# Kernel tuning notes

Hardware: AMD Instinct MI355X
Metric: run time of the kernel (lower is better)

Reference implementation:

```python
import jax, jax.numpy as jnp
import numpy as np

DEPTH = 2
DIM = 1024     # shot-embedding width
SDIM = 256     # SSM state width
B = 256        # batch (episodes x classes)
S = 64         # shots per class (scan length)
EPS = 1e-5


def setup_inputs() -> dict:
    key = jax.random.key(0)
    ks = jax.random.split(key, 10)
    sc = 0.02
    return {
        "shot_embeddings": jax.random.normal(ks[0], (B, S, DIM), jnp.float32),
        # per-layer selective-scan cell params (stacked over depth)
        "Wd": jax.random.normal(ks[1], (DEPTH, DIM, SDIM), jnp.float32) * sc,   # delta proj
        "bd": jnp.zeros((DEPTH, SDIM), jnp.float32),
        "Wi": jax.random.normal(ks[2], (DEPTH, DIM, SDIM), jnp.float32) * sc,   # input (B) proj
        "bi": jnp.zeros((DEPTH, SDIM), jnp.float32),
        "A_log": jax.random.normal(ks[3], (DEPTH, SDIM), jnp.float32),          # state decay param
        "Wo": jax.random.normal(ks[4], (DEPTH, SDIM, DIM), jnp.float32) * sc,   # readout (C) proj
        "bo": jnp.zeros((DEPTH, DIM), jnp.float32),
        # state_to_class Linear(state_dim, dim) per layer
        "Ws": jax.random.normal(ks[5], (DEPTH, SDIM, DIM), jnp.float32) * sc,
        "bs": jnp.zeros((DEPTH, DIM), jnp.float32),
        # LayerNorm
        "gamma": jnp.ones((DIM,), jnp.float32),
        "beta": jnp.zeros((DIM,), jnp.float32),
    }


def _run_selective_scan(x, Wd, bd, Wi, bi, A_log, Wo, bo):
    """Mamba-style selective scan over the shot axis.
    x: [B,S,D] -> (y: [B,S,D], final_state: [B,N])"""
    delta = jax.nn.softplus(jnp.einsum('bsd,dn->bsn', x, Wd) + bd)   # [B,S,N]
    u = jnp.einsum('bsd,dn->bsn', x, Wi) + bi                        # [B,S,N]
    decay = jnp.exp(-delta * jax.nn.softplus(A_log))                 # [B,S,N]
    drive = delta * u                                                # [B,S,N]

    def step(h, t):
        d, g = t
        h = d * h + g
        return h, h

    h0 = jnp.zeros((x.shape[0], Wd.shape[1]), x.dtype)
    final, hs = jax.lax.scan(step, h0, (decay.swapaxes(0, 1), drive.swapaxes(0, 1)))
    hs = hs.swapaxes(0, 1)                                           # [B,S,N]
    y = jnp.einsum('bsn,nd->bsd', hs, Wo) + bo                       # [B,S,D]
    return y, final


def reference(shot_embeddings, Wd, bd, Wi, bi, A_log, Wo, bo, Ws, bs, gamma, beta):
    hidden = shot_embeddings
    class_state = None
    for l in range(Wd.shape[0]):  # fixed small depth
        hidden, state = _run_selective_scan(hidden, Wd[l], bd[l], Wi[l], bi[l],
                                            A_log[l], Wo[l], bo[l])
        class_state = jnp.einsum('bn,nd->bd', state, Ws[l]) + bs[l]   # [B,D]
        hidden = hidden + class_state[:, None, :]
    pooled = class_state + hidden.mean(axis=1)                        # [B,D]
    mu = pooled.mean(axis=-1, keepdims=True)
    var = pooled.var(axis=-1, keepdims=True)
    class_repr = (pooled - mu) / jnp.sqrt(var + EPS) * gamma + beta
    return class_repr, hidden
```

## Files before the change

### kernel.cpp

```cpp
#include <hip/hip_runtime.h>
#include <hip/hip_bf16.h>

#define DEPTH 2
#define DIM   1024
#define SDIM  256
#define BATCH 256
#define SHOTS 64
#define M_TOT (BATCH*SHOTS)
#define SGRP  4
#define GSTEP (SHOTS/SGRP)

typedef __attribute__((ext_vector_type(8))) short bf16x8;
typedef __attribute__((ext_vector_type(4))) float f32x4;
typedef unsigned short u16;

__device__ __forceinline__ u16 f2bf(float f) {
    union { float f; unsigned u; } v; v.f = f;
    unsigned r = v.u + 0x7fffu + ((v.u >> 16) & 1u);
    return (u16)(r >> 16);
}

__device__ __forceinline__ unsigned pk_bf2(float a, float b) {
    union { __hip_bfloat162 h2; unsigned u; } c;
    c.h2 = __float22bfloat162_rn(make_float2(a, b));
    return c.u;
}

__device__ __forceinline__ float softplus_f(float x) {
    if (x > 20.f) return x;
    return log1pf(__expf(x));
}

__device__ __forceinline__ void gld16(const u16* g, u16* l) {
    __builtin_amdgcn_global_load_lds(
        (const __attribute__((address_space(1))) unsigned int*)g,
        (__attribute__((address_space(3))) unsigned int*)l, 16, 0, 0);
}

__global__ __launch_bounds__(256)
void transpose_conv(const float* __restrict__ A1, const float* __restrict__ A2,
                    u16* __restrict__ out, int K, int N, int SPLIT)
{
    __shared__ float T[64][65];
    const int layer = blockIdx.z;
    const int k0 = blockIdx.x * 64, n0 = blockIdx.y * 64;
    const int tid = threadIdx.x;

    const bool first = (n0 < SPLIT);
    const int scols = first ? SPLIT : (N - SPLIT);
    const float* S = (first ? A1 : A2) + (size_t)layer * K * scols
                     + (first ? n0 : (n0 - SPLIT));
    out += (size_t)layer * K * N;

    #pragma unroll
    for (int i = 0; i < 4; ++i) {
        const int c = tid + i * 256;
        const int kr = c >> 4, cc = c & 15;
        const float4 v = *(const float4*)(S + (size_t)(k0 + kr) * scols + cc * 4);
        T[kr][cc * 4 + 0] = v.x; T[kr][cc * 4 + 1] = v.y;
        T[kr][cc * 4 + 2] = v.z; T[kr][cc * 4 + 3] = v.w;
    }
    __syncthreads();
    #pragma unroll
    for (int i = 0; i < 4; ++i) {
        const int c = tid + i * 256;
        const int nr = c >> 4, cc = c & 15;
        ushort4 h;
        h.x = f2bf(T[cc * 4 + 0][nr]); h.y = f2bf(T[cc * 4 + 1][nr]);
        h.z = f2bf(T[cc * 4 + 2][nr]); h.w = f2bf(T[cc * 4 + 3][nr]);
        *(ushort4*)&out[(size_t)(n0 + nr) * K + k0 + cc * 4] = h;
    }
}

__global__ __launch_bounds__(256)
void conv_bf16(const float* __restrict__ in, u16* __restrict__ out)
{
    const size_t total = (size_t)M_TOT * DIM;
    const size_t stride = (size_t)gridDim.x * 256 * 8;
    for (size_t i = ((size_t)blockIdx.x * 256 + threadIdx.x) * 8; i < total; i += stride) {
        const float4 a = *(const float4*)(in + i);
        const float4 b = *(const float4*)(in + i + 4);
        int4 o;
        o.x = (int)pk_bf2(a.x, a.y); o.y = (int)pk_bf2(a.z, a.w);
        o.z = (int)pk_bf2(b.x, b.y); o.w = (int)pk_bf2(b.z, b.w);
        *(int4*)(out + i) = o;
    }
}

#define BM 128
#define BN 128
#define BK 32

template<int EPI, bool SWIZ, bool BF16OUT, bool POOL>
__global__ __launch_bounds__(256)
void gemm_bf16(const u16* __restrict__ A, const u16* __restrict__ BT,
               void* __restrict__ Cv, const float* __restrict__ bo,
               const float* __restrict__ cs, float* __restrict__ pooled,
               int K, int ldc, int CB)
{
    __shared__ __align__(16) u16 As[BM * BK];
    __shared__ __align__(16) u16 Bs[BN * BK];

    const int tid = threadIdx.x;
    const int id  = blockIdx.x;
    int rb, cb;
    if (SWIZ) {
        const int xcd = id & 7, slot = id >> 3;
        rb = xcd + 8 * (slot / CB);
        cb = slot % CB;
    } else {
        rb = id / CB; cb = id % CB;
    }
    const int row0 = rb * BM, col0 = cb * BN;

    const int l  = tid & 63;
    const int w  = tid >> 6;
    const int wm = (w >> 1) * 64, wn = (w & 1) * 64;
    const int lr = l & 15, lq = l >> 4;

    const int sg   = w * 2;
    const int srow = l >> 2;
    const int scol = (l & 3) * 8;
    const u16* Ag = A  + (size_t)(row0 + sg * 16 + srow) * K + scol;
    const u16* Bg = BT + (size_t)(col0 + sg * 16 + srow) * K + scol;
    u16* Asd = &As[sg * 512 + l * 8];
    u16* Bsd = &Bs[sg * 512 + l * 8];

    f32x4 acc[4][4];
    #pragma unroll
    for (int i = 0; i < 4; ++i)
        #pragma unroll
        for (int j = 0; j < 4; ++j)
            acc[i][j] = (f32x4){0.f, 0.f, 0.f, 0.f};

    for (int k0 = 0; k0 < K; k0 += BK) {
        gld16(Ag + k0,                  Asd);
        gld16(Ag + (size_t)16 * K + k0, Asd + 512);
        gld16(Bg + k0,                  Bsd);
        gld16(Bg + (size_t)16 * K + k0, Bsd + 512);
        __syncthreads();

        bf16x8 af[4], bfr[4];
        #pragma unroll
        for (int i = 0; i < 4; ++i)
            af[i] = *(const bf16x8*)&As[(wm + i * 16 + lr) * BK + lq * 8];
        #pragma unroll
        for (int j = 0; j < 4; ++j)
            bfr[j] = *(const bf16x8*)&Bs[(wn + j * 16 + lr) * BK + lq * 8];

        #pragma unroll
        for (int i = 0; i < 4; ++i)
            #pragma unroll
            for (int j = 0; j < 4; ++j)
                acc[i][j] = __builtin_amdgcn_mfma_f32_16x16x32_bf16(
                    af[i], bfr[j], acc[i][j], 0, 0, 0);
        __syncthreads();
    }

    float psum[4] = {0.f, 0.f, 0.f, 0.f};
    #pragma unroll
    for (int i = 0; i < 4; ++i) {
        const int grow = row0 + wm + i * 16 + lq * 4;
        #pragma unroll
        for (int j = 0; j < 4; ++j) {
            const int gcol = col0 + wn + j * 16 + lr;
            float addv = 0.f;
            if (EPI >= 1) addv += bo[gcol];
            if (EPI == 2) addv += cs[(size_t)(grow >> 6) * DIM + gcol];
            #pragma unroll
            for (int r = 0; r < 4; ++r) {
                const float val = acc[i][j][r] + addv;
                if (BF16OUT) ((u16*)Cv)[(size_t)(grow + r) * ldc + gcol] = f2bf(val);
                else         ((float*)Cv)[(size_t)(grow + r) * ldc + gcol] = val;
                if (POOL) psum[j] += val;
            }
        }
    }
    if (POOL) {
        const int batch_w = (row0 + wm) >> 6;
        #pragma unroll
        for (int j = 0; j < 4; ++j) {
            float v = psum[j];
            v += __shfl_xor(v, 16, 64);
            v += __shfl_xor(v, 32, 64);
            if (lq == 0)
                pooled[(size_t)batch_w * DIM + col0 + wn + j * 16 + lr] = v;
        }
    }
}

__global__ __launch_bounds__(512, 8)
void scan_batch(const float* __restrict__ PQ,
                const float* __restrict__ bd, const float* __restrict__ bi,
                const float* __restrict__ A_log,
                u16* __restrict__ hsb, u16* __restrict__ stateb)
{
    const int b  = blockIdx.x;
    const int nc = threadIdx.x & 127;
    const int n  = nc + (blockIdx.y << 7);
    const int g  = threadIdx.x >> 7;
    const float bdv = bd[n], biv = bi[n];
    const float spA = softplus_f(A_log[n]);
    const size_t m0 = (size_t)b * SHOTS + g * GSTEP;
    const float* base = PQ + m0 * 512 + n;

    float dec[GSTEP], drv[GSTEP];
    #pragma unroll
    for (int s = 0; s < GSTEP; ++s) {
        dec[s] = base[s * 512];
        drv[s] = base[s * 512 + SDIM];
    }
    float a = 1.f, hl = 0.f;
    #pragma unroll
    for (int s = 0; s < GSTEP; ++s) {
        const float delta = softplus_f(dec[s] + bdv);
        const float d  = __expf(-delta * spA);
        const float gv = delta * (drv[s] + biv);
        dec[s] = d; drv[s] = gv;
        a *= d; hl = d * hl + gv;
    }

    __shared__ float2 grp[SGRP][128];
    grp[g][nc] = make_float2(a, hl);
    __syncthreads();

    float h = 0.f;
    for (int j = 0; j < g; ++j) {
        const float2 sv = grp[j][nc];
        h = sv.x * h + sv.y;
    }

    u16* hout = hsb + m0 * SDIM + n;
    #pragma unroll
    for (int s = 0; s < GSTEP; ++s) {
        h = dec[s] * h + drv[s];
        hout[s * SDIM] = f2bf(h);
    }
    if (g == SGRP - 1) stateb[(size_t)b * SDIM + n] = f2bf(h);
}

__global__ __launch_bounds__(1024)
void final_kernel(const float* __restrict__ pooled, const float* __restrict__ cs,
                  const float* __restrict__ gamma, const float* __restrict__ beta,
                  float* __restrict__ out)
{
    const int b = blockIdx.x;
    const int d = threadIdx.x;

    const float p = cs[(size_t)b * DIM + d]
                  + pooled[(size_t)b * DIM + d] * (1.f / SHOTS);

    __shared__ float rsum[1024], rsq[1024];
    rsum[d] = p; rsq[d] = p * p;
    __syncthreads();
    for (int off = 512; off > 0; off >>= 1) {
        if (d < off) { rsum[d] += rsum[d + off]; rsq[d] += rsq[d + off]; }
        __syncthreads();
    }
    const float mu  = rsum[0] * (1.f / DIM);
    const float var = rsq[0] * (1.f / DIM) - mu * mu;
    const float inv = rsqrtf(var + 1e-5f);

    out[(size_t)b * DIM + d] = (p - mu) * inv * gamma[d] + beta[d];
}


extern "C" void kernel_launch(void* const* d_in, const int* in_sizes, int n_in,
                              void* d_out, int out_size, void* d_ws, size_t ws_size,
                              hipStream_t stream)
{
    const float* X0    = (const float*)d_in[0];
    const float* Wd    = (const float*)d_in[1];
    const float* bd    = (const float*)d_in[2];
    const float* Wi    = (const float*)d_in[3];
    const float* bi    = (const float*)d_in[4];
    const float* A_log = (const float*)d_in[5];
    const float* Wo    = (const float*)d_in[6];
    const float* bo    = (const float*)d_in[7];
    const float* Ws    = (const float*)d_in[8];
    const float* bs    = (const float*)d_in[9];
    const float* gamma = (const float*)d_in[10];
    const float* beta  = (const float*)d_in[11];

    float* out_cr     = (float*)d_out;
    float* out_hidden = out_cr + (size_t)BATCH * DIM;

    u16* Xbf = (u16*)out_hidden;

    char* w = (char*)d_ws;
    float*  PQ     = (float*)w;  w += (size_t)M_TOT * 512 * 4;
    float*  csbuf  = (float*)w;  w += (size_t)BATCH * DIM * 4;
    float*  pooled = (float*)w;  w += (size_t)BATCH * DIM * 4;
    u16*    stateb = (u16*)w;    w += (size_t)BATCH * SDIM * 2;
    u16*    hsb    = (u16*)w;    w += (size_t)M_TOT * SDIM * 2;
    u16*    WcombT = (u16*)w;    w += (size_t)DEPTH * 512 * 1024 * 2;
    u16*    WoT    = (u16*)w;    w += (size_t)DEPTH * 1024 * 256 * 2;
    u16*    WsT    = (u16*)w;    w += (size_t)DEPTH * 1024 * 256 * 2;

    transpose_conv<<<dim3(1024 / 64, 512 / 64, DEPTH), 256, 0, stream>>>(
        Wd, Wi, WcombT, 1024, 512, 256);
    transpose_conv<<<dim3(256 / 64, 1024 / 64, DEPTH), 256, 0, stream>>>(
        Wo, Wo, WoT, 256, 1024, 1024);
    transpose_conv<<<dim3(256 / 64, 1024 / 64, DEPTH), 256, 0, stream>>>(
        Ws, Ws, WsT, 256, 1024, 1024);
    conv_bf16<<<2048, 256, 0, stream>>>(X0, Xbf);

    for (int l = 0; l < DEPTH; ++l) {
        gemm_bf16<0, true, false, false><<<512, 256, 0, stream>>>(
            Xbf, WcombT + (size_t)l * 512 * 1024, PQ, nullptr, nullptr, nullptr,
            1024, 512, 4);
        scan_batch<<<dim3(BATCH, 2), 512, 0, stream>>>(
            PQ, bd + l * SDIM, bi + l * SDIM, A_log + l * SDIM, hsb, stateb);
        gemm_bf16<1, false, false, false><<<16, 256, 0, stream>>>(
            stateb, WsT + (size_t)l * 1024 * 256, csbuf, bs + l * DIM, nullptr,
            nullptr, 256, 1024, 8);
        if (l < DEPTH - 1) {
            gemm_bf16<2, true, true, false><<<1024, 256, 0, stream>>>(
                hsb, WoT + (size_t)l * 1024 * 256, Xbf, bo + l * DIM, csbuf,
                nullptr, 256, 1024, 8);
        } else {
            gemm_bf16<2, true, false, true><<<1024, 256, 0, stream>>>(
                hsb, WoT + (size_t)l * 1024 * 256, out_hidden, bo + l * DIM, csbuf,
                pooled, 256, 1024, 8);
        }
    }
    final_kernel<<<BATCH, 1024, 0, stream>>>(pooled, csbuf, gamma, beta, out_cr);
}
```

Before: 299.7 us.

## Fuse state-to-class projection into scan kernel and merge prep kernels

Merges the three weight transpose kernels and the input bf16 conversion into a single prep launch. The scan kernel now runs one 1024-thread block per batch item covering all 256 state channels, keeps the final state in shared memory, and computes the state-to-class projection with a scalar dot product over a bf16 copy of Ws. This removes the small 16-block GEMM launch, the stateb round trip and several launches. The cost is that each scan block serially reads a 256x1024 bf16 weight slab, and the scan grid halves, so per-block scalar FMA work and lower parallelism may offset the saved launches.

```diff
diff --git a/kernel.cpp b/kernel.cpp
--- a/kernel.cpp
+++ b/kernel.cpp
@@ -26,6 +26,10 @@
     return c.u;
 }
 
+__device__ __forceinline__ float bf2f(u16 h) {
+    union { unsigned u; float f; } c; c.u = (unsigned)h << 16; return c.f;
+}
+
 __device__ __forceinline__ float softplus_f(float x) {
     if (x > 20.f) return x;
     return log1pf(__expf(x));
@@ -37,15 +41,11 @@
         (__attribute__((address_space(3))) unsigned int*)l, 16, 0, 0);
 }
 
-__global__ __launch_bounds__(256)
-void transpose_conv(const float* __restrict__ A1, const float* __restrict__ A2,
-                    u16* __restrict__ out, int K, int N, int SPLIT)
-{
-    __shared__ float T[64][65];
-    const int layer = blockIdx.z;
-    const int k0 = blockIdx.x * 64, n0 = blockIdx.y * 64;
-    const int tid = threadIdx.x;
-
+__device__ __forceinline__ void transpose_body(
+    float T[64][65], const float* __restrict__ A1, const float* __restrict__ A2,
+    u16* __restrict__ out, int K, int N, int SPLIT, int k0, int n0, int layer,
+    int tid)
+{
     const bool first = (n0 < SPLIT);
     const int scols = first ? SPLIT : (N - SPLIT);
     const float* S = (first ? A1 : A2) + (size_t)layer * K * scols
@@ -73,17 +73,42 @@
 }
 
 __global__ __launch_bounds__(256)
-void conv_bf16(const float* __restrict__ in, u16* __restrict__ out)
-{
-    const size_t total = (size_t)M_TOT * DIM;
-    const size_t stride = (size_t)gridDim.x * 256 * 8;
-    for (size_t i = ((size_t)blockIdx.x * 256 + threadIdx.x) * 8; i < total; i += stride) {
-        const float4 a = *(const float4*)(in + i);
-        const float4 b = *(const float4*)(in + i + 4);
+void prep(const float* __restrict__ Wd, const float* __restrict__ Wi,
+          const float* __restrict__ Wo, const float* __restrict__ Ws,
+          const float* __restrict__ X0,
+          u16* __restrict__ WcombT, u16* __restrict__ WoT,
+          u16* __restrict__ Wsb, u16* __restrict__ Xbf)
+{
+    __shared__ float T[64][65];
+    const int bid = blockIdx.x;
+    const int tid = threadIdx.x;
+
+    if (bid < 256) {
+        const int kx = bid & 15, ny = (bid >> 4) & 7, lz = bid >> 7;
+        transpose_body(T, Wd, Wi, WcombT, 1024, 512, 256, kx * 64, ny * 64, lz, tid);
+    } else if (bid < 384) {
+        const int sub = bid - 256;
+        const int kx = sub & 3, ny = (sub >> 2) & 15, lz = sub >> 6;
+        transpose_body(T, Wo, Wo, WoT, 256, 1024, 1024, kx * 64, ny * 64, lz, tid);
+    } else if (bid < 640) {
+        const size_t i = ((size_t)(bid - 384) * 256 + tid) * 8;
+        const float4 a = *(const float4*)(Ws + i);
+        const float4 b = *(const float4*)(Ws + i + 4);
         int4 o;
         o.x = (int)pk_bf2(a.x, a.y); o.y = (int)pk_bf2(a.z, a.w);
         o.z = (int)pk_bf2(b.x, b.y); o.w = (int)pk_bf2(b.z, b.w);
-        *(int4*)(out + i) = o;
+        *(int4*)(Wsb + i) = o;
+    } else {
+        const size_t total = (size_t)M_TOT * DIM;
+        const size_t stride = (size_t)2048 * 256 * 8;
+        for (size_t i = ((size_t)(bid - 640) * 256 + tid) * 8; i < total; i += stride) {
+            const float4 a = *(const float4*)(X0 + i);
+            const float4 b = *(const float4*)(X0 + i + 4);
+            int4 o;
+            o.x = (int)pk_bf2(a.x, a.y); o.y = (int)pk_bf2(a.z, a.w);
+            o.z = (int)pk_bf2(b.x, b.y); o.w = (int)pk_bf2(b.z, b.w);
+            *(int4*)(Xbf + i) = o;
+        }
     }
 }
 
@@ -189,16 +214,16 @@
     }
 }
 
-__global__ __launch_bounds__(512, 8)
-void scan_batch(const float* __restrict__ PQ,
-                const float* __restrict__ bd, const float* __restrict__ bi,
-                const float* __restrict__ A_log,
-                u16* __restrict__ hsb, u16* __restrict__ stateb)
-{
-    const int b  = blockIdx.x;
-    const int nc = threadIdx.x & 127;
-    const int n  = nc + (blockIdx.y << 7);
-    const int g  = threadIdx.x >> 7;
+__global__ __launch_bounds__(1024)
+void scan_cs(const float* __restrict__ PQ,
+             const float* __restrict__ bd, const float* __restrict__ bi,
+             const float* __restrict__ A_log,
+             const u16* __restrict__ Wsb, const float* __restrict__ bs,
+             u16* __restrict__ hsb, float* __restrict__ csbuf)
+{
+    const int b = blockIdx.x;
+    const int n = threadIdx.x & 255;
+    const int g = threadIdx.x >> 8;
     const float bdv = bd[n], biv = bi[n];
     const float spA = softplus_f(A_log[n]);
     const size_t m0 = (size_t)b * SHOTS + g * GSTEP;
@@ -220,13 +245,14 @@
         a *= d; hl = d * hl + gv;
     }
 
-    __shared__ float2 grp[SGRP][128];
-    grp[g][nc] = make_float2(a, hl);
+    __shared__ float2 grp[SGRP][SDIM];
+    __shared__ float st[SDIM];
+    grp[g][n] = make_float2(a, hl);
     __syncthreads();
 
     float h = 0.f;
     for (int j = 0; j < g; ++j) {
-        const float2 sv = grp[j][nc];
+        const float2 sv = grp[j][n];
         h = sv.x * h + sv.y;
     }
 
@@ -236,7 +262,16 @@
         h = dec[s] * h + drv[s];
         hout[s * SDIM] = f2bf(h);
     }
-    if (g == SGRP - 1) stateb[(size_t)b * SDIM + n] = f2bf(h);
+    if (g == SGRP - 1) st[n] = h;
+    __syncthreads();
+
+    const int d = threadIdx.x;
+    float c = bs[d];
+    const u16* wp = Wsb + d;
+    #pragma unroll 8
+    for (int k = 0; k < SDIM; ++k)
+        c += st[k] * bf2f(wp[(size_t)k * DIM]);
+    csbuf[(size_t)b * DIM + d] = c;
 }
 
 __global__ __launch_bounds__(1024)
@@ -291,29 +326,20 @@
     float*  PQ     = (float*)w;  w += (size_t)M_TOT * 512 * 4;
     float*  csbuf  = (float*)w;  w += (size_t)BATCH * DIM * 4;
     float*  pooled = (float*)w;  w += (size_t)BATCH * DIM * 4;
-    u16*    stateb = (u16*)w;    w += (size_t)BATCH * SDIM * 2;
     u16*    hsb    = (u16*)w;    w += (size_t)M_TOT * SDIM * 2;
     u16*    WcombT = (u16*)w;    w += (size_t)DEPTH * 512 * 1024 * 2;
     u16*    WoT    = (u16*)w;    w += (size_t)DEPTH * 1024 * 256 * 2;
-    u16*    WsT    = (u16*)w;    w += (size_t)DEPTH * 1024 * 256 * 2;
-
-    transpose_conv<<<dim3(1024 / 64, 512 / 64, DEPTH), 256, 0, stream>>>(
-        Wd, Wi, WcombT, 1024, 512, 256);
-    transpose_conv<<<dim3(256 / 64, 1024 / 64, DEPTH), 256, 0, stream>>>(
-        Wo, Wo, WoT, 256, 1024, 1024);
-    transpose_conv<<<dim3(256 / 64, 1024 / 64, DEPTH), 256, 0, stream>>>(
-        Ws, Ws, WsT, 256, 1024, 1024);
-    conv_bf16<<<2048, 256, 0, stream>>>(X0, Xbf);
+    u16*    Wsb    = (u16*)w;    w += (size_t)DEPTH * SDIM * DIM * 2;
+
+    prep<<<2688, 256, 0, stream>>>(Wd, Wi, Wo, Ws, X0, WcombT, WoT, Wsb, Xbf);
 
     for (int l = 0; l < DEPTH; ++l) {
         gemm_bf16<0, true, false, false><<<512, 256, 0, stream>>>(
             Xbf, WcombT + (size_t)l * 512 * 1024, PQ, nullptr, nullptr, nullptr,
             1024, 512, 4);
-        scan_batch<<<dim3(BATCH, 2), 512, 0, stream>>>(
-            PQ, bd + l * SDIM, bi + l * SDIM, A_log + l * SDIM, hsb, stateb);
-        gemm_bf16<1, false, false, false><<<16, 256, 0, stream>>>(
-            stateb, WsT + (size_t)l * 1024 * 256, csbuf, bs + l * DIM, nullptr,
-            nullptr, 256, 1024, 8);
+        scan_cs<<<BATCH, 1024, 0, stream>>>(
+            PQ, bd + l * SDIM, bi + l * SDIM, A_log + l * SDIM,
+            Wsb + (size_t)l * SDIM * DIM, bs + l * DIM, hsb, csbuf);
         if (l < DEPTH - 1) {
             gemm_bf16<2, true, true, false><<<1024, 256, 0, stream>>>(
                 hsb, WoT + (size_t)l * 1024 * 256, Xbf, bo + l * DIM, csbuf,
```

New measurement: 296.5 us. About the same (-1.1%).
